# Performance work log

Hardware: AMD Instinct MI355X
Metric: run time of the kernel (lower is better)

The kernel has to match this reference:

```python
import jax, jax.numpy as jnp
import numpy as np

BIG = 1e11  # torch code replaces zero counts with 1e11 before dividing
N_LABELS = 5


def _label_mean(state, func):
    """Masked mean per label (1..5). state [..., S, H], func [..., S] int.
    Returns aug [..., 5, H], aug_mask [..., 5] bool. Zero-count labels -> 0
    (sum is exactly 0 and denom is BIG, matching the torch zero-init path)."""
    mask = (func[..., None] == jnp.arange(1, N_LABELS + 1)).astype(state.dtype)  # [...,S,5]
    sums = jnp.einsum('...sl,...sh->...lh', mask, state)                          # [...,5,H]
    counts = mask.sum(axis=-2)                                                    # [...,5]
    aug_mask = counts > 0
    denom = jnp.where(aug_mask, counts, jnp.asarray(BIG, state.dtype))
    return sums / denom[..., None], aug_mask


def _masked_mean(state, func):
    """Mean over all non-pad (func != 0) sentences. state [..., S, H]."""
    m = (func != 0).astype(state.dtype)
    s = jnp.einsum('...s,...sh->...h', m, state)
    c = m.sum(axis=-1)
    pm = c > 0
    denom = jnp.where(pm, c, jnp.asarray(BIG, state.dtype))
    return s / denom[..., None], pm


def setup_inputs() -> dict:
    key = jax.random.key(0)
    k1, k2, k3, k4 = jax.random.split(key, 4)
    B, TS, H = 8, 512, 512       # batch, tar_n_sents, enc_hidden_size
    D, RS = 32, 256              # ref_n_docs, ref_n_sents
    return {
        'tarsent_state': jax.random.normal(k1, (B, TS, H), jnp.float32),
        'tar_func': jax.random.randint(k2, (B, TS), 0, 6),
        'refsent_state': jax.random.normal(k3, (B, D, RS, H), jnp.float32),
        'ref_func': jax.random.randint(k4, (B, D, RS), 0, 6),
    }


def reference(tarsent_state, tar_func, refsent_state, ref_func):
    # tar_aug_state [B,5,H], tar_aug_mask [B,5]
    tar_aug, tar_aug_mask = _label_mean(tarsent_state, tar_func)
    # ref_aug_state [B,D,5,H], ref_aug_mask [B,D,5]
    ref_aug, ref_aug_mask = _label_mean(refsent_state, ref_func)
    # tarpaper_state [B,H], refpaper_state [B,D,H]
    tarpaper_state, tar_mask2 = _masked_mean(tarsent_state, tar_func)
    refpaper_state, ref_mask2 = _masked_mean(refsent_state, ref_func)
    return (tar_aug, tar_aug_mask, ref_aug, ref_aug_mask,
            tarpaper_state, tar_mask2, refpaper_state, ref_mask2)
```

## Files before the change

kernel.cpp:

```cpp
#include <hip/hip_runtime.h>


#define H      512
#define HV     128
#define NL     5
#define BIGF   1e11f
#define CHUNK  64
#define RPC    8

#define OFF_TAR_AUG       0
#define OFF_TAR_AUG_MASK  20480
#define OFF_REF_AUG       20520
#define OFF_REF_AUG_MASK  675880
#define OFF_TARPAPER      677160
#define OFF_TAR_MASK2     681256
#define OFF_REFPAPER      681264
#define OFF_REF_MASK2     812336

#define NCHUNK_REF 4
#define NCHUNK_TAR 8
#define NBLK_REF   1024
#define NBLK1      1088
#define WSUM_ELEMS ((size_t)NBLK1 * NL * H)
#define WCNT_OFF_B (WSUM_ELEMS * 4)
#define WS_NEED    (WCNT_OFF_B + (size_t)NBLK1 * NL * 4)

__device__ inline float4 f4add(float4 a, float4 b) {
    a.x += b.x; a.y += b.y; a.z += b.z; a.w += b.w; return a;
}
__device__ inline float4 f4scale(float4 a, float s) {
    a.x *= s; a.y *= s; a.z *= s; a.w *= s; return a;
}
__device__ inline float4 f4fma(float w, float4 v, float4 a) {
    a.x = fmaf(w, v.x, a.x); a.y = fmaf(w, v.y, a.y);
    a.z = fmaf(w, v.z, a.z); a.w = fmaf(w, v.w, a.w); return a;
}
__device__ inline void async_copy16(const float* g, float* l) {
    __builtin_amdgcn_global_load_lds(
        (const __attribute__((address_space(1))) void*)g,
        (__attribute__((address_space(3))) void*)l, 16, 0, 0);
}

__global__ __launch_bounds__(256) void emenc_stage1(
    const float* __restrict__ tar_state, const int* __restrict__ tar_func,
    const float* __restrict__ ref_state, const int* __restrict__ ref_func,
    float* __restrict__ wsum, int* __restrict__ wcnt)
{
    __shared__ float  sbuf[RPC * H];
    __shared__ float4 spart[HV * NL];
    __shared__ int    crow[CHUNK];
    __shared__ int    clab[CHUNK];
    __shared__ int    scnt5[NL];
    __shared__ int    sm;

    const int b = blockIdx.x;
    const float* state;
    const int*   func;
    int s0;
    if (b < NBLK_REF) {
        const int seg = b >> 2, ch = b & 3;
        state = ref_state + (size_t)seg * 256 * H;
        func  = ref_func  + seg * 256;
        s0    = ch * CHUNK;
    } else {
        const int q = b - NBLK_REF;
        const int seg = q >> 3, ch = q & 7;
        state = tar_state + (size_t)seg * 512 * H;
        func  = tar_func  + seg * 512;
        s0    = ch * CHUNK;
    }

    const int tid = threadIdx.x;

    if (tid < CHUNK) {
        const int l = func[s0 + tid];
        #pragma unroll
        for (int q = 1; q <= NL; ++q) {
            const unsigned long long mq = __ballot(l == q);
            if (tid == 0) scnt5[q - 1] = (int)__popcll(mq);
        }
        const unsigned long long mask = __ballot(l != 0);
        if (l != 0) {
            const int pos = (int)__popcll(mask & ((1ull << tid) - 1ull));
            crow[pos] = tid;
            clab[pos] = l;
        }
        if (tid == 0) sm = (int)__popcll(mask);
    }
    __syncthreads();

    const int m     = sm;
    const int col   = tid & (HV - 1);
    const int phase = tid >> 7;
    const int lane  = tid & 63;
    const int wv    = tid >> 6;

    float4 a1 = {0,0,0,0}, a2 = {0,0,0,0}, a3 = {0,0,0,0},
           a4 = {0,0,0,0}, a5 = {0,0,0,0};

    const int nch = (m + RPC - 1) / RPC;
    for (int c = 0; c < nch; ++c) {
        const int r0   = c * RPC;
        const int rem  = m - r0;
        const int rows = rem < RPC ? rem : RPC;

        #pragma unroll
        for (int k = 0; k < 4; ++k) {
            const int j  = wv * 4 + k;
            const int rs = j >> 1;
            if (rs < rows) {
                const int half = j & 1;
                const int row  = crow[r0 + rs];
                const float* g = state + (size_t)(s0 + row) * H
                                 + half * 256 + lane * 4;
                float* l = sbuf + rs * H + half * 256;
                async_copy16(g, l);
            }
        }
        __builtin_amdgcn_s_waitcnt(0xF70);
        __syncthreads();

        for (int r = phase; r < rows; r += 2) {
            const int l = clab[r0 + r];
            const float4 v = *(const float4*)(sbuf + r * H + col * 4);
            a1 = f4fma((l == 1) ? 1.0f : 0.0f, v, a1);
            a2 = f4fma((l == 2) ? 1.0f : 0.0f, v, a2);
            a3 = f4fma((l == 3) ? 1.0f : 0.0f, v, a3);
            a4 = f4fma((l == 4) ? 1.0f : 0.0f, v, a4);
            a5 = f4fma((l == 5) ? 1.0f : 0.0f, v, a5);
        }
        __syncthreads();
    }

    if (phase == 1) {
        spart[col * NL + 0] = a1;
        spart[col * NL + 1] = a2;
        spart[col * NL + 2] = a3;
        spart[col * NL + 3] = a4;
        spart[col * NL + 4] = a5;
    }
    __syncthreads();

    if (phase == 0) {
        a1 = f4add(a1, spart[col * NL + 0]);
        a2 = f4add(a2, spart[col * NL + 1]);
        a3 = f4add(a3, spart[col * NL + 2]);
        a4 = f4add(a4, spart[col * NL + 3]);
        a5 = f4add(a5, spart[col * NL + 4]);

        float* wb = wsum + (size_t)b * NL * H;
        ((float4*)(wb + 0 * H))[col] = a1;
        ((float4*)(wb + 1 * H))[col] = a2;
        ((float4*)(wb + 2 * H))[col] = a3;
        ((float4*)(wb + 3 * H))[col] = a4;
        ((float4*)(wb + 4 * H))[col] = a5;
    }
    if (tid < NL) wcnt[b * NL + tid] = scnt5[tid];
}

__global__ __launch_bounds__(128) void emenc_stage2(
    const float* __restrict__ wsum, const int* __restrict__ wcnt,
    float* __restrict__ out)
{
    const int bb   = blockIdx.x;
    const int seg  = bb / 6;
    const int role = bb - seg * 6;

    int nch, wb0;
    float *aug, *augmask, *paper, *mask2;
    if (seg < 256) {
        nch = NCHUNK_REF; wb0 = seg * NCHUNK_REF;
        aug     = out + OFF_REF_AUG      + (size_t)seg * NL * H;
        augmask = out + OFF_REF_AUG_MASK + seg * NL;
        paper   = out + OFF_REFPAPER     + (size_t)seg * H;
        mask2   = out + OFF_REF_MASK2    + seg;
    } else {
        const int q = seg - 256;
        nch = NCHUNK_TAR; wb0 = NBLK_REF + q * NCHUNK_TAR;
        aug     = out + OFF_TAR_AUG      + (size_t)q * NL * H;
        augmask = out + OFF_TAR_AUG_MASK + q * NL;
        paper   = out + OFF_TARPAPER     + (size_t)q * H;
        mask2   = out + OFF_TAR_MASK2    + q;
    }

    const int col = threadIdx.x;

    if (role < NL) {
        int c = 0;
        for (int ch = 0; ch < nch; ch++) c += wcnt[(wb0 + ch) * NL + role];
        float4 s = {0,0,0,0};
        for (int ch = 0; ch < nch; ch++)
            s = f4add(s, ((const float4*)(wsum + (size_t)(wb0 + ch) * NL * H
                                          + (size_t)role * H))[col]);
        const float inv = 1.0f / (c > 0 ? (float)c : BIGF);
        ((float4*)(aug + (size_t)role * H))[col] = f4scale(s, inv);
        if (col == 0) augmask[role] = c > 0 ? 1.0f : 0.0f;
    } else {
        int ct = 0;
        for (int ch = 0; ch < nch; ch++) {
            #pragma unroll
            for (int l = 0; l < NL; l++) ct += wcnt[(wb0 + ch) * NL + l];
        }
        float4 t = {0,0,0,0};
        for (int ch = 0; ch < nch; ch++) {
            const float4* wb = (const float4*)(wsum + (size_t)(wb0 + ch) * NL * H);
            #pragma unroll
            for (int l = 0; l < NL; l++) t = f4add(t, wb[l * HV + col]);
        }
        ((float4*)paper)[col] = f4scale(t, 1.0f / (ct > 0 ? (float)ct : BIGF));
        if (col == 0) mask2[0] = ct > 0 ? 1.0f : 0.0f;
    }
}

__global__ __launch_bounds__(256) void emenc_single(
    const float* __restrict__ tar_state, const int* __restrict__ tar_func,
    const float* __restrict__ ref_state, const int* __restrict__ ref_func,
    float* __restrict__ out)
{
    __shared__ int    sfunc[512];
    __shared__ float4 spart[HV * NL];
    __shared__ int    scnt[NL];

    const int b = blockIdx.x;
    const float* state;
    const int*   func;
    int S;
    float *aug, *augmask, *paper, *mask2;

    if (b < 256) {
        state   = ref_state + (size_t)b * 256 * H;
        func    = ref_func  + b * 256;
        S       = 256;
        aug     = out + OFF_REF_AUG      + (size_t)b * NL * H;
        augmask = out + OFF_REF_AUG_MASK + b * NL;
        paper   = out + OFF_REFPAPER     + (size_t)b * H;
        mask2   = out + OFF_REF_MASK2    + b;
    } else {
        const int q = b - 256;
        state   = tar_state + (size_t)q * 512 * H;
        func    = tar_func  + q * 512;
        S       = 512;
        aug     = out + OFF_TAR_AUG      + (size_t)q * NL * H;
        augmask = out + OFF_TAR_AUG_MASK + q * NL;
        paper   = out + OFF_TARPAPER     + (size_t)q * H;
        mask2   = out + OFF_TAR_MASK2    + q;
    }

    const int tid = threadIdx.x;
    for (int i = tid; i < S; i += 256) sfunc[i] = func[i];
    __syncthreads();

    const int col   = tid & (HV - 1);
    const int phase = tid >> 7;

    float4 a1 = {0,0,0,0}, a2 = {0,0,0,0}, a3 = {0,0,0,0},
           a4 = {0,0,0,0}, a5 = {0,0,0,0};

    for (int s = phase; s < S; s += 2) {
        float4 v = ((const float4*)(state + (size_t)s * H))[col];
        const int l = sfunc[s];
        a1 = f4fma((l == 1) ? 1.0f : 0.0f, v, a1);
        a2 = f4fma((l == 2) ? 1.0f : 0.0f, v, a2);
        a3 = f4fma((l == 3) ? 1.0f : 0.0f, v, a3);
        a4 = f4fma((l == 4) ? 1.0f : 0.0f, v, a4);
        a5 = f4fma((l == 5) ? 1.0f : 0.0f, v, a5);
    }

    if (phase == 1) {
        spart[col * NL + 0] = a1;
        spart[col * NL + 1] = a2;
        spart[col * NL + 2] = a3;
        spart[col * NL + 3] = a4;
        spart[col * NL + 4] = a5;
    }
    if (tid < NL) {
        int c = 0;
        for (int i = 0; i < S; ++i) c += (sfunc[i] == tid + 1) ? 1 : 0;
        scnt[tid] = c;
    }
    __syncthreads();

    if (phase == 0) {
        a1 = f4add(a1, spart[col * NL + 0]);
        a2 = f4add(a2, spart[col * NL + 1]);
        a3 = f4add(a3, spart[col * NL + 2]);
        a4 = f4add(a4, spart[col * NL + 3]);
        a5 = f4add(a5, spart[col * NL + 4]);

        const int c1 = scnt[0], c2 = scnt[1], c3 = scnt[2],
                  c4 = scnt[3], c5 = scnt[4];
        float4 t  = f4add(f4add(f4add(a1, a2), f4add(a3, a4)), a5);
        const int ct = c1 + c2 + c3 + c4 + c5;

        ((float4*)(aug + 0 * H))[col] = f4scale(a1, 1.0f / (c1 > 0 ? (float)c1 : BIGF));
        ((float4*)(aug + 1 * H))[col] = f4scale(a2, 1.0f / (c2 > 0 ? (float)c2 : BIGF));
        ((float4*)(aug + 2 * H))[col] = f4scale(a3, 1.0f / (c3 > 0 ? (float)c3 : BIGF));
        ((float4*)(aug + 3 * H))[col] = f4scale(a4, 1.0f / (c4 > 0 ? (float)c4 : BIGF));
        ((float4*)(aug + 4 * H))[col] = f4scale(a5, 1.0f / (c5 > 0 ? (float)c5 : BIGF));
        ((float4*)paper)[col]         = f4scale(t,  1.0f / (ct > 0 ? (float)ct : BIGF));

        if (col == 0) {
            augmask[0] = c1 > 0 ? 1.0f : 0.0f;
            augmask[1] = c2 > 0 ? 1.0f : 0.0f;
            augmask[2] = c3 > 0 ? 1.0f : 0.0f;
            augmask[3] = c4 > 0 ? 1.0f : 0.0f;
            augmask[4] = c5 > 0 ? 1.0f : 0.0f;
            mask2[0]   = ct > 0 ? 1.0f : 0.0f;
        }
    }
}

extern "C" void kernel_launch(void* const* d_in, const int* in_sizes, int n_in,
                              void* d_out, int out_size, void* d_ws, size_t ws_size,
                              hipStream_t stream) {
    const float* tar_state = (const float*)d_in[0];
    const int*   tar_func  = (const int*)d_in[1];
    const float* ref_state = (const float*)d_in[2];
    const int*   ref_func  = (const int*)d_in[3];
    float* out = (float*)d_out;

    if (ws_size >= WS_NEED) {
        float* wsum = (float*)d_ws;
        int*   wcnt = (int*)((char*)d_ws + WCNT_OFF_B);
        emenc_stage1<<<NBLK1, 256, 0, stream>>>(tar_state, tar_func,
                                                ref_state, ref_func, wsum, wcnt);
        emenc_stage2<<<264 * 6, 128, 0, stream>>>(wsum, wcnt, out);
    } else {
        emenc_single<<<264, 256, 0, stream>>>(tar_state, tar_func,
                                              ref_state, ref_func, out);
    }
}
```

Baseline: 207.8 us.

## Double-buffer per-wave async row loads and drop block-wide barriers in stage1

Stage 1 now gives each wave its own pair of LDS buffers and has it load 2 rows per step, with the next step's loads issued before the current rows are consumed. Waits use vmcnt counters instead of block-wide __syncthreads, so loading and accumulating overlap within each wave. Each wave holds all 512 columns for 5 labels in registers, and the four waves' partial sums are combined in LDS with a two-level tree at the end. This raises register pressure and adds more LDS traffic in the final reduction. Out-of-range row indices are clamped to the last valid row, so some loads fetch rows that are then discarded.

```diff
diff --git a/kernel.cpp b/kernel.cpp
--- a/kernel.cpp
+++ b/kernel.cpp
@@ -6,7 +6,8 @@
 #define NL     5
 #define BIGF   1e11f
 #define CHUNK  64
-#define RPC    8
+#define RPB    2
+#define NBUF   8
 
 #define OFF_TAR_AUG       0
 #define OFF_TAR_AUG_MASK  20480
@@ -46,12 +47,11 @@
     const float* __restrict__ ref_state, const int* __restrict__ ref_func,
     float* __restrict__ wsum, int* __restrict__ wcnt)
 {
-    __shared__ float  sbuf[RPC * H];
-    __shared__ float4 spart[HV * NL];
-    __shared__ int    crow[CHUNK];
-    __shared__ int    clab[CHUNK];
-    __shared__ int    scnt5[NL];
-    __shared__ int    sm;
+    __shared__ float sbuf[4 * 2 * RPB * 512];
+    __shared__ int   crow[CHUNK];
+    __shared__ int   clab[CHUNK];
+    __shared__ int   scnt5[NL];
+    __shared__ int   sm;
 
     const int b = blockIdx.x;
     const float* state;
@@ -70,7 +70,9 @@
         s0    = ch * CHUNK;
     }
 
-    const int tid = threadIdx.x;
+    const int tid  = threadIdx.x;
+    const int wv   = tid >> 6;
+    const int lane = tid & 63;
 
     if (tid < CHUNK) {
         const int l = func[s0 + tid];
@@ -89,71 +91,108 @@
     }
     __syncthreads();
 
-    const int m     = sm;
-    const int col   = tid & (HV - 1);
-    const int phase = tid >> 7;
-    const int lane  = tid & 63;
-    const int wv    = tid >> 6;
-
-    float4 a1 = {0,0,0,0}, a2 = {0,0,0,0}, a3 = {0,0,0,0},
-           a4 = {0,0,0,0}, a5 = {0,0,0,0};
-
-    const int nch = (m + RPC - 1) / RPC;
-    for (int c = 0; c < nch; ++c) {
-        const int r0   = c * RPC;
-        const int rem  = m - r0;
-        const int rows = rem < RPC ? rem : RPC;
-
-        #pragma unroll
-        for (int k = 0; k < 4; ++k) {
-            const int j  = wv * 4 + k;
-            const int rs = j >> 1;
-            if (rs < rows) {
-                const int half = j & 1;
-                const int row  = crow[r0 + rs];
-                const float* g = state + (size_t)(s0 + row) * H
-                                 + half * 256 + lane * 4;
-                float* l = sbuf + rs * H + half * 256;
-                async_copy16(g, l);
+    const int m = sm;
+
+    float4 acc[NL][2];
+    #pragma unroll
+    for (int l = 0; l < NL; ++l) {
+        acc[l][0] = make_float4(0,0,0,0);
+        acc[l][1] = make_float4(0,0,0,0);
+    }
+
+    if (m > 0) {
+        auto issue = [&](int j) {
+            #pragma unroll
+            for (int r = 0; r < RPB; ++r) {
+                int idx = j * 8 + wv * RPB + r;
+                if (idx >= m) idx = m - 1;
+                const int row = crow[idx];
+                const float* gb = state + (size_t)(s0 + row) * H;
+                float* lb = sbuf + ((wv * 2 + (j & 1)) * RPB + r) * 512;
+                async_copy16(gb + lane * 4, lb);
+                async_copy16(gb + 256 + lane * 4, lb + 256);
             }
-        }
-        __builtin_amdgcn_s_waitcnt(0xF70);
-        __syncthreads();
-
-        for (int r = phase; r < rows; r += 2) {
-            const int l = clab[r0 + r];
-            const float4 v = *(const float4*)(sbuf + r * H + col * 4);
-            a1 = f4fma((l == 1) ? 1.0f : 0.0f, v, a1);
-            a2 = f4fma((l == 2) ? 1.0f : 0.0f, v, a2);
-            a3 = f4fma((l == 3) ? 1.0f : 0.0f, v, a3);
-            a4 = f4fma((l == 4) ? 1.0f : 0.0f, v, a4);
-            a5 = f4fma((l == 5) ? 1.0f : 0.0f, v, a5);
-        }
-        __syncthreads();
-    }
-
-    if (phase == 1) {
-        spart[col * NL + 0] = a1;
-        spart[col * NL + 1] = a2;
-        spart[col * NL + 2] = a3;
-        spart[col * NL + 3] = a4;
-        spart[col * NL + 4] = a5;
-    }
-    __syncthreads();
-
-    if (phase == 0) {
-        a1 = f4add(a1, spart[col * NL + 0]);
-        a2 = f4add(a2, spart[col * NL + 1]);
-        a3 = f4add(a3, spart[col * NL + 2]);
-        a4 = f4add(a4, spart[col * NL + 3]);
-        a5 = f4add(a5, spart[col * NL + 4]);
-
+        };
+
+        issue(0);
+        issue(1);
+
+        #pragma unroll
+        for (int j = 0; j < NBUF; ++j) {
+            if (j < NBUF - 1) asm volatile("s_waitcnt vmcnt(4)" ::: "memory");
+            else              asm volatile("s_waitcnt vmcnt(0)" ::: "memory");
+
+            const float* lb = sbuf + (wv * 2 + (j & 1)) * RPB * 512;
+            #pragma unroll
+            for (int r = 0; r < RPB; ++r) {
+                const int idx = j * 8 + wv * RPB + r;
+                if (idx < m) {
+                    const int l = clab[idx];
+                    const float w1 = (l == 1) ? 1.0f : 0.0f;
+                    const float w2 = (l == 2) ? 1.0f : 0.0f;
+                    const float w3 = (l == 3) ? 1.0f : 0.0f;
+                    const float w4 = (l == 4) ? 1.0f : 0.0f;
+                    const float w5 = (l == 5) ? 1.0f : 0.0f;
+                    const float4 v0 = *(const float4*)(lb + r * 512 + lane * 4);
+                    const float4 v1 = *(const float4*)(lb + r * 512 + 256 + lane * 4);
+                    acc[0][0] = f4fma(w1, v0, acc[0][0]);
+                    acc[0][1] = f4fma(w1, v1, acc[0][1]);
+                    acc[1][0] = f4fma(w2, v0, acc[1][0]);
+                    acc[1][1] = f4fma(w2, v1, acc[1][1]);
+                    acc[2][0] = f4fma(w3, v0, acc[2][0]);
+                    acc[2][1] = f4fma(w3, v1, acc[2][1]);
+                    acc[3][0] = f4fma(w4, v0, acc[3][0]);
+                    acc[3][1] = f4fma(w4, v1, acc[3][1]);
+                    acc[4][0] = f4fma(w5, v0, acc[4][0]);
+                    acc[4][1] = f4fma(w5, v1, acc[4][1]);
+                }
+            }
+            if (j + 2 < NBUF) {
+                asm volatile("" ::: "memory");
+                issue(j + 2);
+            }
+        }
+    }
+
+    __syncthreads();
+    float* flat = sbuf;
+    if (wv >= 2) {
+        float* dst = flat + (wv - 2) * (NL * 512);
+        #pragma unroll
+        for (int l = 0; l < NL; ++l) {
+            *(float4*)(dst + l * 512 + lane * 4)       = acc[l][0];
+            *(float4*)(dst + l * 512 + 256 + lane * 4) = acc[l][1];
+        }
+    }
+    __syncthreads();
+    if (wv < 2) {
+        const float* src = flat + wv * (NL * 512);
+        #pragma unroll
+        for (int l = 0; l < NL; ++l) {
+            acc[l][0] = f4add(acc[l][0], *(const float4*)(src + l * 512 + lane * 4));
+            acc[l][1] = f4add(acc[l][1], *(const float4*)(src + l * 512 + 256 + lane * 4));
+        }
+    }
+    __syncthreads();
+    if (wv == 1) {
+        float* dst = flat;
+        #pragma unroll
+        for (int l = 0; l < NL; ++l) {
+            *(float4*)(dst + l * 512 + lane * 4)       = acc[l][0];
+            *(float4*)(dst + l * 512 + 256 + lane * 4) = acc[l][1];
+        }
+    }
+    __syncthreads();
+    if (wv == 0) {
+        const float* src = flat;
         float* wb = wsum + (size_t)b * NL * H;
-        ((float4*)(wb + 0 * H))[col] = a1;
-        ((float4*)(wb + 1 * H))[col] = a2;
-        ((float4*)(wb + 2 * H))[col] = a3;
-        ((float4*)(wb + 3 * H))[col] = a4;
-        ((float4*)(wb + 4 * H))[col] = a5;
+        #pragma unroll
+        for (int l = 0; l < NL; ++l) {
+            float4 s0v = f4add(acc[l][0], *(const float4*)(src + l * 512 + lane * 4));
+            float4 s1v = f4add(acc[l][1], *(const float4*)(src + l * 512 + 256 + lane * 4));
+            *(float4*)(wb + l * H + lane * 4)       = s0v;
+            *(float4*)(wb + l * H + 256 + lane * 4) = s1v;
+        }
     }
     if (tid < NL) wcnt[b * NL + tid] = scnt5[tid];
 }
```

Measured after the change: 208.5 us. About the same (+0.3%).
